# Optimization experiments

Hardware: AMD Instinct MI355X
Metric: run time of the kernel (lower is better)

Reference implementation:

```python
import jax, jax.numpy as jnp
import numpy as np

EPS = 1e-12

def _prelu(x, a):
    return jnp.where(x >= 0, x, a * x)

def _l2norm(x):
    n = jnp.sqrt(jnp.sum(x * x, axis=1, keepdims=True))
    return x / jnp.maximum(n, EPS)

def setup_inputs() -> dict:
    key = jax.random.key(0)
    ks = jax.random.split(key, 8)
    N, E, F_IN, F_OUT = 262144, 4194304, 128, 64
    feat = jax.random.normal(ks[0], (N, F_IN), dtype=jnp.float32)
    edge_src = jax.random.randint(ks[1], (E,), 0, N, dtype=jnp.int32)
    edge_dst = jax.random.randint(ks[2], (E,), 0, N, dtype=jnp.int32)
    edge_w = jax.random.uniform(ks[3], (E,), dtype=jnp.float32)
    # Glorot-uniform projection weight, zero biases (reset_parameters)
    lim = float(np.sqrt(6.0 / (F_IN + F_OUT)))
    weight = jax.random.uniform(ks[4], (F_IN, F_OUT), minval=-lim, maxval=lim, dtype=jnp.float32)
    bias = jnp.zeros((F_OUT,), dtype=jnp.float32)
    prelu_a = jnp.full((1,), 0.25, dtype=jnp.float32)
    lim2 = float(np.sqrt(1.0 / F_OUT))  # torch Linear default init range
    w_sub = jax.random.uniform(ks[5], (F_OUT, F_OUT), minval=-lim2, maxval=lim2, dtype=jnp.float32)
    b_sub = jnp.zeros((F_OUT,), dtype=jnp.float32)
    w_gcn = jax.random.uniform(ks[6], (F_OUT, F_OUT), minval=-lim2, maxval=lim2, dtype=jnp.float32)
    b_gcn = jnp.zeros((F_OUT,), dtype=jnp.float32)
    return {"feat": feat, "edge_src": edge_src, "edge_dst": edge_dst, "edge_w": edge_w,
            "weight": weight, "bias": bias, "prelu_a": prelu_a,
            "w_sub": w_sub, "b_sub": b_sub, "w_gcn": w_gcn, "b_gcn": b_gcn}

def reference(feat, edge_src, edge_dst, edge_w, weight, bias, prelu_a,
              w_sub, b_sub, w_gcn, b_gcn):
    N = feat.shape[0]
    G = N // 4  # 4 nodes per subgraph, anchors at stride 4
    # anchor rows extracted, then zeroed in the feature matrix (in-place in torch)
    anchor_embs = feat[::4, :]
    feat_z = feat.at[::4, :].set(0.0)
    anchor_out = _prelu(anchor_embs @ weight + bias, prelu_a)
    # GraphConv(norm='none', weight=False, bias=False) with edge weights:
    # h[dst] = sum_e w_e * (feat_z @ W)[src_e]
    in_feat = feat_z @ weight                      # [N, F_OUT]
    msgs = in_feat[edge_src] * edge_w[:, None]     # [E, F_OUT]
    h = jax.ops.segment_sum(msgs, edge_dst, num_segments=N)
    h = _prelu(h + bias, prelu_a)
    # AvgPooling per graph (each graph has exactly 4 nodes)
    seg = jnp.arange(N, dtype=jnp.int32) // 4
    subgraph_pool_emb = jax.ops.segment_sum(h, seg, num_segments=G) / 4.0
    gcn_emb = h[::4, :]
    subgraph_pool_emb = subgraph_pool_emb @ w_sub.T + b_sub
    gcn_emb = gcn_emb @ w_gcn.T + b_gcn
    return (_l2norm(subgraph_pool_emb), _l2norm(anchor_out), _l2norm(gcn_emb))
```

## Files before the change

### kernel.cpp

```cpp
#include <hip/hip_runtime.h>
#include <hip/hip_fp16.h>

#define EPSN 1e-12f
#define NBC  256
#define RBF  1024
#define CHK  8192
#define NWGMAX 1024
#define GU   16
#define WQS  16384.0f

typedef _Float16 half8_t __attribute__((ext_vector_type(8)));
typedef float    f32x4  __attribute__((ext_vector_type(4)));

__device__ __forceinline__ float rdlane(float v, int k) {
    return __int_as_float(__builtin_amdgcn_readlane(__float_as_int(v), k));
}
__device__ __forceinline__ float preluf(float x, float a) {
    return x >= 0.0f ? x : a * x;
}

__global__ __launch_bounds__(256) void k_mfma(
    const float* __restrict__ feat, const float* __restrict__ weight,
    const float* __restrict__ bias, const float* __restrict__ prelu_a,
    __half* __restrict__ in_feat, float* __restrict__ out_anchor,
    int N, int totalWaves)
{
    const int lane = threadIdx.x & 63;
    const int r    = lane & 15;
    const int g    = lane >> 4;
    const int wid  = (int)((blockIdx.x * (size_t)blockDim.x + threadIdx.x) >> 6);
    const int nt4  = N >> 4;

    half8_t bfr[4][4];
    #pragma unroll
    for (int nt = 0; nt < 4; ++nt)
        #pragma unroll
        for (int kq = 0; kq < 4; ++kq)
            #pragma unroll
            for (int e = 0; e < 8; ++e)
                bfr[nt][kq][e] =
                    (_Float16)weight[(kq * 32 + g * 8 + e) * 64 + nt * 16 + r];

    float bj[4];
    #pragma unroll
    for (int nt = 0; nt < 4; ++nt) bj[nt] = bias[nt * 16 + r];
    const float a = prelu_a[0];

    for (int t = wid; t < nt4; t += totalWaves) {
        const int rb = t << 4;

        f32x4 acc[4];
        #pragma unroll
        for (int nt = 0; nt < 4; ++nt) acc[nt] = (f32x4){0.f, 0.f, 0.f, 0.f};

        const float* fr = feat + (size_t)(rb + r) * 128 + g * 8;
        #pragma unroll
        for (int kq = 0; kq < 4; ++kq) {
            const float4 f0 = *(const float4*)(fr + kq * 32);
            const float4 f1 = *(const float4*)(fr + kq * 32 + 4);
            half8_t af;
            af[0] = (_Float16)f0.x; af[1] = (_Float16)f0.y;
            af[2] = (_Float16)f0.z; af[3] = (_Float16)f0.w;
            af[4] = (_Float16)f1.x; af[5] = (_Float16)f1.y;
            af[6] = (_Float16)f1.z; af[7] = (_Float16)f1.w;
            #pragma unroll
            for (int nt = 0; nt < 4; ++nt)
                acc[nt] = __builtin_amdgcn_mfma_f32_16x16x32_f16(
                    af, bfr[nt][kq], acc[nt], 0, 0, 0);
        }

        const int row0 = rb + g * 4;
        float ss = 0.0f, y[4];
        #pragma unroll
        for (int nt = 0; nt < 4; ++nt) {
            y[nt] = preluf(acc[nt][0] + bj[nt], a);
            ss = fmaf(y[nt], y[nt], ss);
        }
        ss += __shfl_xor(ss, 1, 16);
        ss += __shfl_xor(ss, 2, 16);
        ss += __shfl_xor(ss, 4, 16);
        ss += __shfl_xor(ss, 8, 16);
        const float inv = 1.0f / fmaxf(sqrtf(ss), EPSN);
        #pragma unroll
        for (int nt = 0; nt < 4; ++nt)
            out_anchor[(size_t)(row0 >> 2) * 64 + nt * 16 + r] = y[nt] * inv;
        #pragma unroll
        for (int nt = 0; nt < 4; ++nt)
            in_feat[(size_t)row0 * 64 + nt * 16 + r] = __float2half(0.0f);
        #pragma unroll
        for (int reg = 1; reg < 4; ++reg)
            #pragma unroll
            for (int nt = 0; nt < 4; ++nt)
                in_feat[(size_t)(row0 + reg) * 64 + nt * 16 + r] =
                    __float2half(acc[nt][reg]);
    }
}

__global__ __launch_bounds__(256) void k_transform2(
    const float* __restrict__ feat, const float* __restrict__ weight,
    const float* __restrict__ bias, const float* __restrict__ prelu_a,
    __half* __restrict__ in_feat, float* __restrict__ out_anchor,
    int N, int totalWaves)
{
    const int lane  = threadIdx.x & 63;
    const int wid   = (int)((blockIdx.x * (size_t)blockDim.x + threadIdx.x) >> 6);
    const int tiles = (N + 63) >> 6;

    for (int tile = wid; tile < tiles; tile += totalWaves) {
        const int row = tile * 64 + lane;
        if (row >= N) continue;

        float acc[64];
        #pragma unroll
        for (int j = 0; j < 64; ++j) acc[j] = 0.0f;

        const float4* fp = (const float4*)(feat + (size_t)row * 128);
        #pragma unroll 4
        for (int kc = 0; kc < 32; ++kc) {
            const float4 f = fp[kc];
            const float fs[4] = {f.x, f.y, f.z, f.w};
            #pragma unroll
            for (int kk = 0; kk < 4; ++kk) {
                const float fv = fs[kk];
                const float* wr = weight + (kc * 4 + kk) * 64;
                #pragma unroll
                for (int j = 0; j < 64; ++j)
                    acc[j] = fmaf(fv, wr[j], acc[j]);
            }
        }

        if ((row & 3) == 0) {
            const float a = prelu_a[0];
            float ss = 0.0f;
            #pragma unroll
            for (int j = 0; j < 64; ++j) {
                acc[j] = preluf(acc[j] + bias[j], a);
                ss = fmaf(acc[j], acc[j], ss);
            }
            const float inv = 1.0f / fmaxf(sqrtf(ss), EPSN);
            float* ap = out_anchor + (size_t)(row >> 2) * 64;
            #pragma unroll
            for (int j = 0; j < 64; ++j) ap[j] = acc[j] * inv;
            #pragma unroll
            for (int j = 0; j < 64; ++j)
                in_feat[(size_t)row * 64 + j] = __float2half(0.0f);
        } else {
            #pragma unroll
            for (int j = 0; j < 64; ++j)
                in_feat[(size_t)row * 64 + j] = __float2half(acc[j]);
        }
    }
}

__global__ __launch_bounds__(256) void s_count2(
    const int* __restrict__ esrc, const int* __restrict__ edst, int E,
    unsigned* __restrict__ C)
{
    __shared__ unsigned hist[NBC];
    const int t = threadIdx.x;
    hist[t] = 0;
    __syncthreads();
    const int base = blockIdx.x * CHK;
    for (int r = 0; r < CHK / (16 * 256); ++r) {
        int d[16];
        #pragma unroll
        for (int i = 0; i < 16; ++i) {
            const int idx = base + (r * 16 + i) * 256 + t;
            d[i] = -1;
            if (idx < E) {
                const int s = esrc[idx];
                if ((s & 3) != 0) d[i] = edst[idx];
            }
        }
        #pragma unroll
        for (int i = 0; i < 16; ++i)
            if (d[i] >= 0) atomicAdd(&hist[((unsigned)d[i]) >> 10], 1u);
    }
    __syncthreads();
    C[(size_t)blockIdx.x * NBC + t] = hist[t];
}

__global__ __launch_bounds__(256) void s_scanA(
    unsigned* __restrict__ C, unsigned* __restrict__ T, int nwg)
{
    __shared__ unsigned ssum[256];
    const int i = blockIdx.x;
    const int t = threadIdx.x;
    const int PER = (nwg + 255) / 256;
    unsigned vals[4];
    unsigned run = 0;
    for (int p = 0; p < PER; ++p) {
        const int blk = t * PER + p;
        const unsigned v = (blk < nwg) ? C[(size_t)blk * NBC + i] : 0u;
        vals[p] = run;
        run += v;
    }
    ssum[t] = run;
    __syncthreads();
    for (int off = 1; off < 256; off <<= 1) {
        unsigned x = (t >= off) ? ssum[t - off] : 0u;
        __syncthreads();
        ssum[t] += x;
        __syncthreads();
    }
    const unsigned texcl = ssum[t] - run;
    for (int p = 0; p < PER; ++p) {
        const int blk = t * PER + p;
        if (blk < nwg) C[(size_t)blk * NBC + i] = texcl + vals[p];
    }
    if (t == 255) T[i] = ssum[255];
}

__global__ __launch_bounds__(256) void s_scanB(
    const unsigned* __restrict__ T, unsigned* __restrict__ basep,
    unsigned* __restrict__ rs, int N)
{
    __shared__ unsigned sc[NBC];
    const int t = threadIdx.x;
    const unsigned my = T[t];
    sc[t] = my;
    __syncthreads();
    for (int off = 1; off < NBC; off <<= 1) {
        unsigned a = (t >= off) ? sc[t - off] : 0u;
        __syncthreads();
        sc[t] += a;
        __syncthreads();
    }
    basep[t] = sc[t] - my;
    if (t == NBC - 1) { basep[NBC] = sc[t]; rs[N] = sc[t]; }
}

__global__ __launch_bounds__(256) void s_scatter4(
    const int* __restrict__ esrc, const int* __restrict__ edst,
    const float* __restrict__ ew, int E,
    const unsigned* __restrict__ basep, const unsigned* __restrict__ C,
    const unsigned* __restrict__ T, int nwg,
    uint2* __restrict__ recs)
{
    __shared__ uint2    buf[CHK];
    __shared__ unsigned cur[NBC];
    __shared__ unsigned cb [NBC];
    __shared__ unsigned ssum[256];
    const int blk = blockIdx.x;
    const int t   = threadIdx.x;

    const unsigned own = C[(size_t)blk * NBC + t];
    const unsigned nxt = (blk + 1 < nwg) ? C[(size_t)(blk + 1) * NBC + t] : T[t];
    const unsigned myc = nxt - own;
    ssum[t] = myc;
    __syncthreads();
    for (int off = 1; off < 256; off <<= 1) {
        unsigned x = (t >= off) ? ssum[t - off] : 0u;
        __syncthreads();
        ssum[t] += x;
        __syncthreads();
    }
    const unsigned excl = ssum[t] - myc;
    cur[t] = excl;
    cb[t]  = basep[t] + own - excl;
    __syncthreads();
    const unsigned cnt = ssum[255];

    const int base = blk * CHK;
    for (int r = 0; r < CHK / (16 * 256); ++r) {
        int s[16], d[16]; float wv[16];
        #pragma unroll
        for (int i = 0; i < 16; ++i) {
            const int idx = base + (r * 16 + i) * 256 + t;
            const bool ok = (idx < E);
            s[i]  = ok ? esrc[idx] : 0;
            d[i]  = ok ? edst[idx] : 0;
            wv[i] = ok ? ew[idx]   : 0.0f;
            if (!ok || (s[i] & 3) == 0) d[i] = -1;
        }
        #pragma unroll
        for (int i = 0; i < 16; ++i) {
            if (d[i] >= 0) {
                const unsigned slot = atomicAdd(&cur[((unsigned)d[i]) >> 10], 1u);
                const unsigned wq =
                    min((unsigned)(wv[i] * WQS + 0.5f), 16383u);
                buf[slot] = make_uint2(((unsigned)s[i]) | (wq << 18),
                                       (unsigned)d[i]);
            }
        }
    }
    __syncthreads();
    for (unsigned i = t; i < cnt; i += 256) {
        const uint2 rr = buf[i];
        recs[cb[rr.y >> 10] + i] = rr;
    }
}

__global__ __launch_bounds__(256) void s_sortfine(
    const uint2* __restrict__ recs, const unsigned* __restrict__ basep,
    unsigned* __restrict__ recf, unsigned* __restrict__ rs)
{
    __shared__ unsigned hist[RBF], cur[RBF], ssum[256];
    const int t = threadIdx.x;
    const int b = blockIdx.x;
    const unsigned start = basep[b], end = basep[b + 1];
    #pragma unroll
    for (int p = 0; p < 4; ++p) hist[t * 4 + p] = 0;
    __syncthreads();
    for (unsigned i = start + t; i < end; i += 256)
        atomicAdd(&hist[recs[i].y & (RBF - 1u)], 1u);
    __syncthreads();
    unsigned vals[4], run = 0;
    #pragma unroll
    for (int p = 0; p < 4; ++p) { vals[p] = run; run += hist[t * 4 + p]; }
    ssum[t] = run;
    __syncthreads();
    for (int off = 1; off < 256; off <<= 1) {
        unsigned x = (t >= off) ? ssum[t - off] : 0u;
        __syncthreads();
        ssum[t] += x;
        __syncthreads();
    }
    const unsigned texcl = ssum[t] - run;
    #pragma unroll
    for (int p = 0; p < 4; ++p) {
        const int i = t * 4 + p;
        const unsigned e = start + texcl + vals[p];
        cur[i] = e;
        rs[b * RBF + i] = e;
    }
    __syncthreads();
    for (unsigned i = start + t; i < end; i += 256) {
        const uint2 r = recs[i];
        const unsigned slot = atomicAdd(&cur[r.y & (RBF - 1u)], 1u);
        recf[slot] = r.x;
    }
}

__global__ __launch_bounds__(256) void s_accum4(
    const __half* __restrict__ in_feat, const unsigned* __restrict__ recf,
    const unsigned* __restrict__ rs, float* __restrict__ h,
    int NROWS, int totalWaves)
{
    const int lane = threadIdx.x & 63;
    const int wid = (int)((blockIdx.x * (size_t)blockDim.x + threadIdx.x) >> 6);

    for (int row = wid; row < NROWS; row += totalWaves) {
        const unsigned s = rs[row], e = rs[row + 1];
        float acc = 0.0f;
        unsigned done = s;
        while (done < e) {
            const int c = (int)min(64u, e - done);
            unsigned rcd = 0u;
            if (lane < c) rcd = recf[done + lane];
            for (int j0 = 0; j0 < c; j0 += GU) {
                float v[GU], wj[GU];
                #pragma unroll
                for (int jj = 0; jj < GU; ++jj) {
                    const int idx = j0 + jj;
                    const int cl  = (idx < c) ? idx : (c - 1);
                    const unsigned px =
                        (unsigned)__builtin_amdgcn_readlane((int)rcd, cl);
                    v[jj]  = __half2float(
                        in_feat[((size_t)(px & 0x3FFFFu) << 6) + lane]);
                    wj[jj] = (idx < c) ? (float)(px >> 18) : 0.0f;
                }
                #pragma unroll
                for (int jj = 0; jj < GU; ++jj) acc = fmaf(v[jj], wj[jj], acc);
            }
            done += (unsigned)c;
        }
        h[((size_t)row << 6) + lane] = acc * (1.0f / WQS);
    }
}

#define K2_U 8
__global__ __launch_bounds__(256) void k_edges(
    const __half* __restrict__ in_feat, const int* __restrict__ esrc,
    const int* __restrict__ edst, const float* __restrict__ ew,
    float* __restrict__ h, int E, int totalWaves)
{
    const int lane = threadIdx.x & 63;
    int wid = (int)((blockIdx.x * (size_t)blockDim.x + threadIdx.x) >> 6);
    wid = __builtin_amdgcn_readfirstlane(wid);
    const int chunk = (E + totalWaves - 1) / totalWaves;
    int e0 = wid * chunk;
    int e1 = min(e0 + chunk, E);
    for (int base = e0; base < e1; base += K2_U) {
        const int nb = min(K2_U, e1 - base);
        int s[K2_U], d[K2_U]; float w[K2_U];
        #pragma unroll
        for (int j = 0; j < K2_U; ++j) {
            int idx = base + ((j < nb) ? j : 0);
            s[j] = esrc[idx]; d[j] = edst[idx]; w[j] = ew[idx];
        }
        float v[K2_U];
        #pragma unroll
        for (int j = 0; j < K2_U; ++j)
            v[j] = __half2float(in_feat[((size_t)s[j] << 6) + lane]);
        #pragma unroll
        for (int j = 0; j < K2_U; ++j)
            if (j < nb) atomicAdd(h + ((size_t)d[j] << 6) + lane, v[j] * w[j]);
    }
}

__global__ __launch_bounds__(256) void k_finalize(
    const float* __restrict__ h, const float* __restrict__ bias,
    const float* __restrict__ prelu_a,
    const float* __restrict__ w_sub, const float* __restrict__ b_sub,
    const float* __restrict__ w_gcn, const float* __restrict__ b_gcn,
    float* __restrict__ out_sub, float* __restrict__ out_gcn,
    int G, int totalWaves)
{
    const int lane = threadIdx.x & 63;
    const int wid = (int)((blockIdx.x * (size_t)blockDim.x + threadIdx.x) >> 6);

    float wsreg[64], wgreg[64];
    #pragma unroll
    for (int k = 0; k < 64; ++k) wsreg[k] = w_sub[lane * 64 + k];
    #pragma unroll
    for (int k = 0; k < 64; ++k) wgreg[k] = w_gcn[lane * 64 + k];
    const float bj  = bias[lane];
    const float bsj = b_sub[lane];
    const float bgj = b_gcn[lane];
    const float a   = prelu_a[0];

    for (int g = wid; g < G; g += totalWaves) {
        const float* hp = h + (size_t)g * 256;
        float p0 = preluf(hp[lane]       + bj, a);
        float p1 = preluf(hp[64  + lane] + bj, a);
        float p2 = preluf(hp[128 + lane] + bj, a);
        float p3 = preluf(hp[192 + lane] + bj, a);
        float pool = (p0 + p1 + p2 + p3) * 0.25f;
        float gcn  = p0;

        float as = bsj, ag = bgj;
        #pragma unroll
        for (int k = 0; k < 64; ++k) {
            as = fmaf(rdlane(pool, k), wsreg[k], as);
            ag = fmaf(rdlane(gcn,  k), wgreg[k], ag);
        }
        float ss = as * as, sg = ag * ag;
        #pragma unroll
        for (int off = 32; off >= 1; off >>= 1) {
            ss += __shfl_xor(ss, off, 64);
            sg += __shfl_xor(sg, off, 64);
        }
        out_sub[(size_t)g * 64 + lane] = as / fmaxf(sqrtf(ss), EPSN);
        out_gcn[(size_t)g * 64 + lane] = ag / fmaxf(sqrtf(sg), EPSN);
    }
}

extern "C" void kernel_launch(void* const* d_in, const int* in_sizes, int n_in,
                              void* d_out, int out_size, void* d_ws, size_t ws_size,
                              hipStream_t stream)
{
    const float* feat    = (const float*)d_in[0];
    const int*   esrc    = (const int*)  d_in[1];
    const int*   edst    = (const int*)  d_in[2];
    const float* ew      = (const float*)d_in[3];
    const float* weight  = (const float*)d_in[4];
    const float* bias    = (const float*)d_in[5];
    const float* prelu_a = (const float*)d_in[6];
    const float* w_sub   = (const float*)d_in[7];
    const float* b_sub   = (const float*)d_in[8];
    const float* w_gcn   = (const float*)d_in[9];
    const float* b_gcn   = (const float*)d_in[10];

    const int N = in_sizes[0] / 128;
    const int E = in_sizes[1];
    const int G = N / 4;
    const int nwg = (E + CHK - 1) / CHK;

    char* wsb = (char*)d_ws;
    const size_t AH    = (size_t)N * 64 * 2;
    const size_t A     = (size_t)N * 64 * 4;
    const size_t offRf = AH + A;
    const size_t offC  = offRf + (size_t)E * 4;
    const size_t offT  = offC  + (size_t)nwg * NBC * 4;
    const size_t offBp = offT  + (size_t)NBC * 4;
    const size_t offRs = offBp + (size_t)(NBC + 1) * 4;
    const size_t ws_need = offRs + (size_t)(N + 1) * 4;

    __half*   in_feat = (__half*)wsb;
    float*    h       = (float*)(wsb + AH);
    uint2*    recs    = (uint2*)(wsb + AH);
    unsigned* recf    = (unsigned*)(wsb + offRf);
    unsigned* C       = (unsigned*)(wsb + offC);
    unsigned* T       = (unsigned*)(wsb + offT);
    unsigned* basep   = (unsigned*)(wsb + offBp);
    unsigned* rs      = (unsigned*)(wsb + offRs);

    float* out        = (float*)d_out;
    float* out_sub    = out;
    float* out_anchor = out + (size_t)G * 64;
    float* out_gcn    = out + (size_t)2 * G * 64;

    const bool sorted_path =
        (N == NBC * RBF) && (nwg <= NWGMAX) && ((size_t)E * 8 <= A) &&
        (ws_size >= ws_need);

    {
        const int blocks = 1024, tw = blocks * 4;
        if ((N & 15) == 0)
            k_mfma<<<blocks, 256, 0, stream>>>(feat, weight, bias, prelu_a,
                                               in_feat, out_anchor, N, tw);
        else
            k_transform2<<<blocks, 256, 0, stream>>>(feat, weight, bias, prelu_a,
                                                     in_feat, out_anchor, N, tw);
    }

    if (sorted_path) {
        s_count2  <<<nwg, 256, 0, stream>>>(esrc, edst, E, C);
        s_scanA   <<<NBC, 256, 0, stream>>>(C, T, nwg);
        s_scanB   <<<1, 256, 0, stream>>>(T, basep, rs, N);
        s_scatter4<<<nwg, 256, 0, stream>>>(esrc, edst, ew, E, basep, C, T,
                                            nwg, recs);
        s_sortfine<<<NBC, 256, 0, stream>>>(recs, basep, recf, rs);
        {
            const int blocks = 2048, tw = blocks * 4;
            s_accum4<<<blocks, 256, 0, stream>>>(in_feat, recf, rs, h, N, tw);
        }
        {
            const int blocks = 4096, tw = blocks * 4;
            k_finalize<<<blocks, 256, 0, stream>>>(h, bias, prelu_a, w_sub, b_sub,
                                                   w_gcn, b_gcn, out_sub, out_gcn, G, tw);
        }
    } else if (ws_size >= AH + A) {
        hipMemsetAsync(h, 0, A, stream);
        const int blocks = 2048, tw = blocks * 4;
        k_edges<<<blocks, 256, 0, stream>>>(in_feat, esrc, edst, ew, h, E, tw);
        const int fblocks = 4096, ftw = fblocks * 4;
        k_finalize<<<fblocks, 256, 0, stream>>>(h, bias, prelu_a, w_sub, b_sub,
                                                w_gcn, b_gcn, out_sub, out_gcn, G, ftw);
    }
}
```

Baseline: 518.7 us.

## Fuse transform with edge counting, drop scanB kernel, widen accumulation gathers

Merges the MFMA feature transform and the destination-bucket counting into one launch, with the two jobs split by block index so they run concurrently. Removes the single-block scanB kernel by having scatter and sortfine each recompute the 256-entry bucket prefix locally. Rewrites the accumulation kernel so each lane loads a half2 covering two columns and the two half-waves process alternating edges, then combines them with a cross-half shuffle. This trades redundant small scans and some extra shuffle work for fewer launches and wider loads. The fallback path now uses only the scalar transform kernel, since k_mfma was folded into k_tc.

Measured after the change: 481.4 us. -7.2%, faster.

```diff
diff --git a/kernel.cpp b/kernel.cpp
--- a/kernel.cpp
+++ b/kernel.cpp
@@ -6,7 +6,7 @@
 #define RBF  1024
 #define CHK  8192
 #define NWGMAX 1024
-#define GU   16
+#define PU   4
 #define WQS  16384.0f
 
 typedef _Float16 half8_t __attribute__((ext_vector_type(8)));
@@ -19,16 +19,15 @@
     return x >= 0.0f ? x : a * x;
 }
 
-__global__ __launch_bounds__(256) void k_mfma(
+__device__ __forceinline__ void transform_body(
     const float* __restrict__ feat, const float* __restrict__ weight,
     const float* __restrict__ bias, const float* __restrict__ prelu_a,
     __half* __restrict__ in_feat, float* __restrict__ out_anchor,
-    int N, int totalWaves)
+    int N, int wid, int totalWaves)
 {
     const int lane = threadIdx.x & 63;
     const int r    = lane & 15;
     const int g    = lane >> 4;
-    const int wid  = (int)((blockIdx.x * (size_t)blockDim.x + threadIdx.x) >> 6);
     const int nt4  = N >> 4;
 
     half8_t bfr[4][4];
@@ -96,71 +95,26 @@
     }
 }
 
-__global__ __launch_bounds__(256) void k_transform2(
+__global__ __launch_bounds__(256) void k_tc(
     const float* __restrict__ feat, const float* __restrict__ weight,
     const float* __restrict__ bias, const float* __restrict__ prelu_a,
-    __half* __restrict__ in_feat, float* __restrict__ out_anchor,
-    int N, int totalWaves)
-{
-    const int lane  = threadIdx.x & 63;
-    const int wid   = (int)((blockIdx.x * (size_t)blockDim.x + threadIdx.x) >> 6);
-    const int tiles = (N + 63) >> 6;
-
-    for (int tile = wid; tile < tiles; tile += totalWaves) {
-        const int row = tile * 64 + lane;
-        if (row >= N) continue;
-
-        float acc[64];
-        #pragma unroll
-        for (int j = 0; j < 64; ++j) acc[j] = 0.0f;
-
-        const float4* fp = (const float4*)(feat + (size_t)row * 128);
-        #pragma unroll 4
-        for (int kc = 0; kc < 32; ++kc) {
-            const float4 f = fp[kc];
-            const float fs[4] = {f.x, f.y, f.z, f.w};
-            #pragma unroll
-            for (int kk = 0; kk < 4; ++kk) {
-                const float fv = fs[kk];
-                const float* wr = weight + (kc * 4 + kk) * 64;
-                #pragma unroll
-                for (int j = 0; j < 64; ++j)
-                    acc[j] = fmaf(fv, wr[j], acc[j]);
-            }
-        }
-
-        if ((row & 3) == 0) {
-            const float a = prelu_a[0];
-            float ss = 0.0f;
-            #pragma unroll
-            for (int j = 0; j < 64; ++j) {
-                acc[j] = preluf(acc[j] + bias[j], a);
-                ss = fmaf(acc[j], acc[j], ss);
-            }
-            const float inv = 1.0f / fmaxf(sqrtf(ss), EPSN);
-            float* ap = out_anchor + (size_t)(row >> 2) * 64;
-            #pragma unroll
-            for (int j = 0; j < 64; ++j) ap[j] = acc[j] * inv;
-            #pragma unroll
-            for (int j = 0; j < 64; ++j)
-                in_feat[(size_t)row * 64 + j] = __float2half(0.0f);
-        } else {
-            #pragma unroll
-            for (int j = 0; j < 64; ++j)
-                in_feat[(size_t)row * 64 + j] = __float2half(acc[j]);
-        }
-    }
-}
-
-__global__ __launch_bounds__(256) void s_count2(
+    __half* __restrict__ in_feat, float* __restrict__ out_anchor, int N,
+    int nbT, int twT,
     const int* __restrict__ esrc, const int* __restrict__ edst, int E,
     unsigned* __restrict__ C)
 {
     __shared__ unsigned hist[NBC];
     const int t = threadIdx.x;
+    if ((int)blockIdx.x < nbT) {
+        const int wid = (int)((blockIdx.x * (size_t)blockDim.x + t) >> 6);
+        transform_body(feat, weight, bias, prelu_a, in_feat, out_anchor,
+                       N, wid, twT);
+        return;
+    }
+    const int blk = (int)blockIdx.x - nbT;
     hist[t] = 0;
     __syncthreads();
-    const int base = blockIdx.x * CHK;
+    const int base = blk * CHK;
     for (int r = 0; r < CHK / (16 * 256); ++r) {
         int d[16];
         #pragma unroll
@@ -177,7 +131,7 @@
             if (d[i] >= 0) atomicAdd(&hist[((unsigned)d[i]) >> 10], 1u);
     }
     __syncthreads();
-    C[(size_t)blockIdx.x * NBC + t] = hist[t];
+    C[(size_t)blk * NBC + t] = hist[t];
 }
 
 __global__ __launch_bounds__(256) void s_scanA(
@@ -211,30 +165,10 @@
     if (t == 255) T[i] = ssum[255];
 }
 
-__global__ __launch_bounds__(256) void s_scanB(
-    const unsigned* __restrict__ T, unsigned* __restrict__ basep,
-    unsigned* __restrict__ rs, int N)
-{
-    __shared__ unsigned sc[NBC];
-    const int t = threadIdx.x;
-    const unsigned my = T[t];
-    sc[t] = my;
-    __syncthreads();
-    for (int off = 1; off < NBC; off <<= 1) {
-        unsigned a = (t >= off) ? sc[t - off] : 0u;
-        __syncthreads();
-        sc[t] += a;
-        __syncthreads();
-    }
-    basep[t] = sc[t] - my;
-    if (t == NBC - 1) { basep[NBC] = sc[t]; rs[N] = sc[t]; }
-}
-
 __global__ __launch_bounds__(256) void s_scatter4(
     const int* __restrict__ esrc, const int* __restrict__ edst,
     const float* __restrict__ ew, int E,
-    const unsigned* __restrict__ basep, const unsigned* __restrict__ C,
-    const unsigned* __restrict__ T, int nwg,
+    const unsigned* __restrict__ C, const unsigned* __restrict__ T, int nwg,
     uint2* __restrict__ recs)
 {
     __shared__ uint2    buf[CHK];
@@ -244,8 +178,20 @@
     const int blk = blockIdx.x;
     const int t   = threadIdx.x;
 
+    const unsigned Tt = T[t];
+    ssum[t] = Tt;
+    __syncthreads();
+    for (int off = 1; off < 256; off <<= 1) {
+        unsigned x = (t >= off) ? ssum[t - off] : 0u;
+        __syncthreads();
+        ssum[t] += x;
+        __syncthreads();
+    }
+    const unsigned basepl = ssum[t] - Tt;
+    __syncthreads();
+
     const unsigned own = C[(size_t)blk * NBC + t];
-    const unsigned nxt = (blk + 1 < nwg) ? C[(size_t)(blk + 1) * NBC + t] : T[t];
+    const unsigned nxt = (blk + 1 < nwg) ? C[(size_t)(blk + 1) * NBC + t] : Tt;
     const unsigned myc = nxt - own;
     ssum[t] = myc;
     __syncthreads();
@@ -257,7 +203,7 @@
     }
     const unsigned excl = ssum[t] - myc;
     cur[t] = excl;
-    cb[t]  = basep[t] + own - excl;
+    cb[t]  = basepl + own - excl;
     __syncthreads();
     const unsigned cnt = ssum[255];
 
@@ -292,13 +238,27 @@
 }
 
 __global__ __launch_bounds__(256) void s_sortfine(
-    const uint2* __restrict__ recs, const unsigned* __restrict__ basep,
-    unsigned* __restrict__ recf, unsigned* __restrict__ rs)
+    const uint2* __restrict__ recs, const unsigned* __restrict__ T,
+    unsigned* __restrict__ recf, unsigned* __restrict__ rs, int N)
 {
     __shared__ unsigned hist[RBF], cur[RBF], ssum[256];
     const int t = threadIdx.x;
     const int b = blockIdx.x;
-    const unsigned start = basep[b], end = basep[b + 1];
+
+    const unsigned Tt = T[t];
+    ssum[t] = Tt;
+    __syncthreads();
+    for (int off = 1; off < 256; off <<= 1) {
+        unsigned x = (t >= off) ? ssum[t - off] : 0u;
+        __syncthreads();
+        ssum[t] += x;
+        __syncthreads();
+    }
+    const unsigned start = (b == 0) ? 0u : ssum[b - 1];
+    const unsigned end   = ssum[b];
+    if (b == NBC - 1 && t == 0) rs[N] = ssum[NBC - 1];
+    __syncthreads();
+
     #pragma unroll
     for (int p = 0; p < 4; ++p) hist[t * 4 + p] = 0;
     __syncthreads();
@@ -332,40 +292,113 @@
     }
 }
 
-__global__ __launch_bounds__(256) void s_accum4(
+__global__ __launch_bounds__(256) void s_accum5(
     const __half* __restrict__ in_feat, const unsigned* __restrict__ recf,
     const unsigned* __restrict__ rs, float* __restrict__ h,
     int NROWS, int totalWaves)
 {
-    const int lane = threadIdx.x & 63;
+    const char* ifb  = (const char*)in_feat;
+    const int   lane = threadIdx.x & 63;
+    const int   l32  = lane & 31;
+    const int   hsel = lane >> 5;
+    const unsigned colb = (unsigned)l32 * 4u;
     const int wid = (int)((blockIdx.x * (size_t)blockDim.x + threadIdx.x) >> 6);
 
     for (int row = wid; row < NROWS; row += totalWaves) {
         const unsigned s = rs[row], e = rs[row + 1];
-        float acc = 0.0f;
-        unsigned done = s;
-        while (done < e) {
+        float acc0 = 0.0f, acc1 = 0.0f;
+        for (unsigned done = s; done < e; done += 64u) {
             const int c = (int)min(64u, e - done);
             unsigned rcd = 0u;
             if (lane < c) rcd = recf[done + lane];
-            for (int j0 = 0; j0 < c; j0 += GU) {
-                float v[GU], wj[GU];
+            const int pairs = (c + 1) >> 1;
+            for (int p0 = 0; p0 < pairs; p0 += PU) {
+                unsigned px[PU];
+                __half2  hh[PU];
+                float    wj[PU];
                 #pragma unroll
-                for (int jj = 0; jj < GU; ++jj) {
-                    const int idx = j0 + jj;
-                    const int cl  = (idx < c) ? idx : (c - 1);
-                    const unsigned px =
-                        (unsigned)__builtin_amdgcn_readlane((int)rcd, cl);
-                    v[jj]  = __half2float(
-                        in_feat[((size_t)(px & 0x3FFFFu) << 6) + lane]);
-                    wj[jj] = (idx < c) ? (float)(px >> 18) : 0.0f;
+                for (int pp = 0; pp < PU; ++pp) {
+                    const int jv = (p0 + pp) * 2 + hsel;
+                    px[pp] = (unsigned)__shfl((int)rcd, jv, 64);
                 }
                 #pragma unroll
-                for (int jj = 0; jj < GU; ++jj) acc = fmaf(v[jj], wj[jj], acc);
+                for (int pp = 0; pp < PU; ++pp) {
+                    const unsigned voff =
+                        ((px[pp] & 0x3FFFFu) << 7) + colb;
+                    hh[pp] = *(const __half2*)(ifb + (size_t)voff);
+                    wj[pp] = (float)(px[pp] >> 18);
+                }
+                #pragma unroll
+                for (int pp = 0; pp < PU; ++pp) {
+                    acc0 = fmaf(__half2float(__low2half(hh[pp])),  wj[pp], acc0);
+                    acc1 = fmaf(__half2float(__high2half(hh[pp])), wj[pp], acc1);
+                }
             }
-            done += (unsigned)c;
-        }
-        h[((size_t)row << 6) + lane] = acc * (1.0f / WQS);
+        }
+        acc0 += __shfl_xor(acc0, 32, 64);
+        acc1 += __shfl_xor(acc1, 32, 64);
+        if (hsel == 0) {
+            float2 o;
+            o.x = acc0 * (1.0f / WQS);
+            o.y = acc1 * (1.0f / WQS);
+            *(float2*)(h + ((size_t)row << 6) + 2 * l32) = o;
+        }
+    }
+}
+
+__global__ __launch_bounds__(256) void k_transform2(
+    const float* __restrict__ feat, const float* __restrict__ weight,
+    const float* __restrict__ bias, const float* __restrict__ prelu_a,
+    __half* __restrict__ in_feat, float* __restrict__ out_anchor,
+    int N, int totalWaves)
+{
+    const int lane  = threadIdx.x & 63;
+    const int wid   = (int)((blockIdx.x * (size_t)blockDim.x + threadIdx.x) >> 6);
+    const int tiles = (N + 63) >> 6;
+
+    for (int tile = wid; tile < tiles; tile += totalWaves) {
+        const int row = tile * 64 + lane;
+        if (row >= N) continue;
+
+        float acc[64];
+        #pragma unroll
+        for (int j = 0; j < 64; ++j) acc[j] = 0.0f;
+
+        const float4* fp = (const float4*)(feat + (size_t)row * 128);
+        #pragma unroll 4
+        for (int kc = 0; kc < 32; ++kc) {
+            const float4 f = fp[kc];
+            const float fs[4] = {f.x, f.y, f.z, f.w};
+            #pragma unroll
+            for (int kk = 0; kk < 4; ++kk) {
+                const float fv = fs[kk];
+                const float* wr = weight + (kc * 4 + kk) * 64;
+                #pragma unroll
+                for (int j = 0; j < 64; ++j)
+                    acc[j] = fmaf(fv, wr[j], acc[j]);
+            }
+        }
+
+        if ((row & 3) == 0) {
+            const float a = prelu_a[0];
+            float ss = 0.0f;
+            #pragma unroll
+            for (int j = 0; j < 64; ++j) {
+                acc[j] = preluf(acc[j] + bias[j], a);
+                ss = fmaf(acc[j], acc[j], ss);
+            }
+            const float inv = 1.0f / fmaxf(sqrtf(ss), EPSN);
+            float* ap = out_anchor + (size_t)(row >> 2) * 64;
+            #pragma unroll
+            for (int j = 0; j < 64; ++j) ap[j] = acc[j] * inv;
+            #pragma unroll
+            for (int j = 0; j < 64; ++j)
+                in_feat[(size_t)row * 64 + j] = __float2half(0.0f);
+        } else {
+            #pragma unroll
+            for (int j = 0; j < 64; ++j)
+                in_feat[(size_t)row * 64 + j] = __float2half(acc[j]);
+        }
     }
 }
 
@@ -473,8 +506,7 @@
     const size_t offRf = AH + A;
     const size_t offC  = offRf + (size_t)E * 4;
     const size_t offT  = offC  + (size_t)nwg * NBC * 4;
-    const size_t offBp = offT  + (size_t)NBC * 4;
-    const size_t offRs = offBp + (size_t)(NBC + 1) * 4;
+    const size_t offRs = offT  + (size_t)NBC * 4;
     const size_t ws_need = offRs + (size_t)(N + 1) * 4;
 
     __half*   in_feat = (__half*)wsb;
@@ -483,7 +515,6 @@
     unsigned* recf    = (unsigned*)(wsb + offRf);
     unsigned* C       = (unsigned*)(wsb + offC);
     unsigned* T       = (unsigned*)(wsb + offT);
-    unsigned* basep   = (unsigned*)(wsb + offBp);
     unsigned* rs      = (unsigned*)(wsb + offRs);
 
     float* out        = (float*)d_out;
@@ -495,26 +526,19 @@
         (N == NBC * RBF) && (nwg <= NWGMAX) && ((size_t)E * 8 <= A) &&
         (ws_size >= ws_need);
 
-    {
-        const int blocks = 1024, tw = blocks * 4;
-        if ((N & 15) == 0)
-            k_mfma<<<blocks, 256, 0, stream>>>(feat, weight, bias, prelu_a,
-                                               in_feat, out_anchor, N, tw);
-        else
-            k_transform2<<<blocks, 256, 0, stream>>>(feat, weight, bias, prelu_a,
-                                                     in_feat, out_anchor, N, tw);
-    }
-
     if (sorted_path) {
-        s_count2  <<<nwg, 256, 0, stream>>>(esrc, edst, E, C);
+        {
+            const int nbT = 1024, twT = nbT * 4;
+            k_tc<<<nbT + nwg, 256, 0, stream>>>(feat, weight, bias, prelu_a,
+                                                in_feat, out_anchor, N, nbT, twT,
+                                                esrc, edst, E, C);
+        }
         s_scanA   <<<NBC, 256, 0, stream>>>(C, T, nwg);
-        s_scanB   <<<1, 256, 0, stream>>>(T, basep, rs, N);
-        s_scatter4<<<nwg, 256, 0, stream>>>(esrc, edst, ew, E, basep, C, T,
-                                            nwg, recs);
-        s_sortfine<<<NBC, 256, 0, stream>>>(recs, basep, recf, rs);
+        s_scatter4<<<nwg, 256, 0, stream>>>(esrc, edst, ew, E, C, T, nwg, recs);
+        s_sortfine<<<NBC, 256, 0, stream>>>(recs, T, recf, rs, N);
         {
             const int blocks = 2048, tw = blocks * 4;
-            s_accum4<<<blocks, 256, 0, stream>>>(in_feat, recf, rs, h, N, tw);
+            s_accum5<<<blocks, 256, 0, stream>>>(in_feat, recf, rs, h, N, tw);
         }
         {
             const int blocks = 4096, tw = blocks * 4;
@@ -522,6 +546,11 @@
                                                    w_gcn, b_gcn, out_sub, out_gcn, G, tw);
         }
     } else if (ws_size >= AH + A) {
+        {
+            const int blocks = 1024, tw = blocks * 4;
+            k_transform2<<<blocks, 256, 0, stream>>>(feat, weight, bias, prelu_a,
+                                                     in_feat, out_anchor, N, tw);
+        }
         hipMemsetAsync(h, 0, A, stream);
         const int blocks = 2048, tw = blocks * 4;
         k_edges<<<blocks, 256, 0, stream>>>(in_feat, esrc, edst, ew, h, E, tw);
```
